# Optimization experiments

Measured on AMD Instinct MI355X. Metric: run time of the kernel, lower is better.

## Reference

```python
import jax, jax.numpy as jnp
import numpy as np

HEADS, MAX_SEQ, N_STATE = 8, 2048, 512
DEPTH = N_STATE // HEADS
B, S = 2, 2048
EPS = 1e-5


def setup_inputs() -> dict:
    key = jax.random.key(0)
    ks = jax.random.split(key, 8)
    sd = lambda f: 1.0 / np.sqrt(f)
    causal = jnp.tril(jnp.ones((S, S), dtype=bool))
    mask = jnp.where(causal, 0.0, -1e9).astype(jnp.float32)[None, None]
    return {
        "x": jax.random.normal(ks[0], (B, S, N_STATE), jnp.float32),
        "mask": mask,
        "W_qkv": jax.random.normal(ks[1], (N_STATE, 3 * N_STATE), jnp.float32) * sd(N_STATE),
        "b_qkv": jnp.zeros((3 * N_STATE,), jnp.float32),
        "W_proj": jax.random.normal(ks[2], (N_STATE, N_STATE), jnp.float32) * sd(N_STATE),
        "b_proj": jnp.zeros((N_STATE,), jnp.float32),
        "E": jax.random.normal(ks[3], (HEADS, MAX_SEQ, DEPTH), jnp.float32) * sd(DEPTH),
        "g1": jnp.ones((N_STATE,), jnp.float32),
        "be1": jnp.zeros((N_STATE,), jnp.float32),
        "g2": jnp.ones((N_STATE,), jnp.float32),
        "be2": jnp.zeros((N_STATE,), jnp.float32),
        "W_fc1": jax.random.normal(ks[4], (N_STATE, 4 * N_STATE), jnp.float32) * sd(N_STATE),
        "b_fc1": jnp.zeros((4 * N_STATE,), jnp.float32),
        "W_fc2": jax.random.normal(ks[5], (4 * N_STATE, N_STATE), jnp.float32) * sd(4 * N_STATE),
        "b_fc2": jnp.zeros((N_STATE,), jnp.float32),
    }


def _layernorm(x, g, b):
    mu = jnp.mean(x, axis=-1, keepdims=True)
    var = jnp.mean(jnp.square(x - mu), axis=-1, keepdims=True)
    return (x - mu) * jax.lax.rsqrt(var + EPS) * g + b


def _relative_skew(rel):
    # rel: [B, H, S, S] = q @ E_slice^T ; skew trick -> relative positions
    b, h, s, _ = rel.shape
    rel = jnp.pad(rel, ((0, 0), (0, 0), (0, 0), (1, 0)))  # [B,H,S,S+1]
    rel = rel.reshape(b, h, s + 1, s)
    return rel[:, :, 1:, :]  # [B,H,S,S]


def reference(x, mask, W_qkv, b_qkv, W_proj, b_proj, E, g1, be1, g2, be2,
              W_fc1, b_fc1, W_fc2, b_fc2):
    b, s, _ = x.shape
    a = _layernorm(x, g1, be1)
    qkv = a @ W_qkv + b_qkv  # [B,S,3N]
    q, k, v = jnp.split(qkv, 3, axis=-1)
    split = lambda t: t.reshape(b, s, HEADS, DEPTH).transpose(0, 2, 1, 3)  # [B,H,S,D]
    q, k, v = split(q), split(k), split(v)
    present = jnp.stack([k, v], axis=1)  # [B,2,H,S,D]

    w = jnp.einsum("bhqd,bhkd->bhqk", q, k)
    E_s = E[:, MAX_SEq if False else MAX_SEQ - s:, :]  # [H,S,D]
    rel = jnp.einsum("bhqd,hld->bhql", q, E_s)
    w = (w + _relative_skew(rel)) * (1.0 / np.sqrt(DEPTH))
    w = w + mask
    w = jax.nn.softmax(w, axis=-1)
    att = jnp.einsum("bhqk,bhkd->bhqd", w, v)
    att = att.transpose(0, 2, 1, 3).reshape(b, s, N_STATE)
    att = att @ W_proj + b_proj

    x = x + att
    m = _layernorm(x, g2, be2)
    m = jax.nn.gelu(m @ W_fc1 + b_fc1) @ W_fc2 + b_fc2
    x = x + m
    return (x, present)
```

## Files before the change

### kernel.cpp

```cpp
#include <hip/hip_runtime.h>
#include <stdint.h>

#define DEV __device__ __forceinline__
#define SCHEDB __builtin_amdgcn_sched_barrier(0)
#define WAITVM(n) asm volatile("s_waitcnt vmcnt(" #n ")" ::: "memory")
#define WAITLG asm volatile("s_waitcnt lgkmcnt(0)" ::: "memory")

typedef __attribute__((ext_vector_type(8))) short bf16x8;
typedef __attribute__((ext_vector_type(4))) float f32x4;

DEV ushort f2bf(float f) {
  union { float f; uint32_t u; } c; c.f = f;
  return (ushort)((c.u + 0x7FFFu + ((c.u >> 16) & 1)) >> 16);
}
DEV bf16x8 ld8(const ushort* p) { return *reinterpret_cast<const bf16x8*>(p); }

DEV void gload16(const void* g, void* l) {
  __builtin_amdgcn_global_load_lds(
      (const __attribute__((address_space(1))) uint32_t*)g,
      (__attribute__((address_space(3))) uint32_t*)l, 16, 0, 0);
}

__global__ __launch_bounds__(256) void k_transpose_bf(const float* __restrict__ in,
                                                      ushort* __restrict__ out,
                                                      int R, int C) {
  __shared__ float t[32][33];
  int tx = threadIdx.x & 31, ty = threadIdx.x >> 5;
  int c0 = blockIdx.x * 32, r0 = blockIdx.y * 32;
#pragma unroll
  for (int k = 0; k < 4; ++k)
    t[ty + 8 * k][tx] = in[(size_t)(r0 + ty + 8 * k) * C + c0 + tx];
  __syncthreads();
#pragma unroll
  for (int k = 0; k < 4; ++k)
    out[(size_t)(c0 + ty + 8 * k) * R + r0 + tx] = f2bf(t[tx][ty + 8 * k]);
}

__global__ __launch_bounds__(256) void k_cvt_bf(const float* __restrict__ in,
                                                ushort* __restrict__ out, int n4) {
  int i = blockIdx.x * 256 + threadIdx.x;
  if (i >= n4) return;
  float4 v = reinterpret_cast<const float4*>(in)[i];
  ushort4 o; o.x = f2bf(v.x); o.y = f2bf(v.y); o.z = f2bf(v.z); o.w = f2bf(v.w);
  reinterpret_cast<ushort4*>(out)[i] = o;
}

__global__ __launch_bounds__(256) void k_ln(const float* __restrict__ x,
                                            const float* __restrict__ g,
                                            const float* __restrict__ be,
                                            ushort* __restrict__ out) {
  int w = threadIdx.x >> 6, lane = threadIdx.x & 63;
  int row = blockIdx.x * 4 + w;
  const float* xr = x + (size_t)row * 512 + lane * 8;
  float4 a = *reinterpret_cast<const float4*>(xr);
  float4 b = *reinterpret_cast<const float4*>(xr + 4);
  float xs[8] = {a.x, a.y, a.z, a.w, b.x, b.y, b.z, b.w};
  float s = 0.f, q = 0.f;
#pragma unroll
  for (int i = 0; i < 8; ++i) { s += xs[i]; q += xs[i] * xs[i]; }
#pragma unroll
  for (int off = 32; off; off >>= 1) { s += __shfl_xor(s, off); q += __shfl_xor(q, off); }
  float mu = s * (1.f / 512.f);
  float var = q * (1.f / 512.f) - mu * mu;
  float inv = rsqrtf(var + 1e-5f);
  const float* gp = g + lane * 8;
  const float* bp = be + lane * 8;
  ushort o[8];
#pragma unroll
  for (int i = 0; i < 8; ++i) o[i] = f2bf((xs[i] - mu) * inv * gp[i] + bp[i]);
  *reinterpret_cast<uint4*>(out + (size_t)row * 512 + lane * 8) = *reinterpret_cast<uint4*>(o);
}

template <int EPI, int BN>
__global__ __launch_bounds__(256) void k_gemm(
    const ushort* __restrict__ A, const ushort* __restrict__ Bt,
    int M, int N, int K,
    const float* __restrict__ bias, const float* __restrict__ res,
    float* __restrict__ outf, ushort* __restrict__ outb,
    float* __restrict__ present, ushort* __restrict__ qbf,
    ushort* __restrict__ kbf, ushort* __restrict__ vtbf) {
  constexpr int NF = BN / 32;
  constexpr int LOADS = 4 + BN / 32;
  __shared__ ushort As[2][128][64];
  __shared__ ushort Bs[2][BN][64];
  const int tid = threadIdx.x, lane = tid & 63, w = tid >> 6;
  const int g = lane >> 4, l16 = lane & 15;
  const int m0 = blockIdx.y * 128, n0 = blockIdx.x * BN;
  const int wm = (w >> 1) * 64, wn = (w & 1) * (BN / 2);
  f32x4 acc[4][NF];
#pragma unroll
  for (int i = 0; i < 4; ++i)
#pragma unroll
    for (int j = 0; j < NF; ++j) acc[i][j] = (f32x4){0.f, 0.f, 0.f, 0.f};

  const int lrow_off = (lane << 4);
  auto stage = [&](int buf, int k0) {
#pragma unroll
    for (int sw = 0; sw < 4; ++sw) {
      int offb = sw * 4096 + w * 1024;
      int loff = offb + lrow_off;
      int row = loff >> 7, colb = loff & 127;
      gload16((const char*)A + (((size_t)(m0 + row) * K + k0) << 1) + colb,
              (char*)(&As[buf][0][0]) + offb);
    }
#pragma unroll
    for (int sw = 0; sw < BN / 32; ++sw) {
      int offb = sw * 4096 + w * 1024;
      int loff = offb + lrow_off;
      int row = loff >> 7, colb = loff & 127;
      gload16((const char*)Bt + (((size_t)(n0 + row) * K + k0) << 1) + colb,
              (char*)(&Bs[buf][0][0]) + offb);
    }
  };

  const int nt = K >> 6;
  stage(0, 0);
  stage(1, 64);
  if constexpr (LOADS == 8) WAITVM(8); else WAITVM(6);
  SCHEDB;
  __builtin_amdgcn_s_barrier();
  SCHEDB;

  for (int t = 0; t < nt; ++t) {
    const int cur = t & 1;
    bf16x8 af[2][4], bfr[2][NF];
#pragma unroll
    for (int kk = 0; kk < 2; ++kk) {
#pragma unroll
      for (int f = 0; f < 4; ++f)
        af[kk][f] = *reinterpret_cast<const bf16x8*>(
            &As[cur][wm + f * 16 + l16][kk * 32 + g * 8]);
#pragma unroll
      for (int f = 0; f < NF; ++f)
        bfr[kk][f] = *reinterpret_cast<const bf16x8*>(
            &Bs[cur][wn + f * 16 + l16][kk * 32 + g * 8]);
    }
    WAITLG;
    SCHEDB;
    __builtin_amdgcn_s_barrier();
    SCHEDB;
    if (t + 2 < nt) stage(cur, (t + 2) << 6);
    SCHEDB;
#pragma unroll
    for (int kk = 0; kk < 2; ++kk)
#pragma unroll
      for (int i = 0; i < 4; ++i)
#pragma unroll
        for (int j = 0; j < NF; ++j)
          acc[i][j] = __builtin_amdgcn_mfma_f32_16x16x32_bf16(
              af[kk][i], bfr[kk][j], acc[i][j], 0, 0, 0);
    SCHEDB;
    if (t + 1 < nt) {
      if (t + 2 < nt) {
        if constexpr (LOADS == 8) WAITVM(8); else WAITVM(6);
      } else {
        WAITVM(0);
      }
      SCHEDB;
      __builtin_amdgcn_s_barrier();
      SCHEDB;
    }
  }

#pragma unroll
  for (int i = 0; i < 4; ++i)
#pragma unroll
    for (int j = 0; j < NF; ++j)
#pragma unroll
      for (int r = 0; r < 4; ++r) {
        int row = m0 + wm + i * 16 + g * 4 + r;
        int col = n0 + wn + j * 16 + l16;
        float v = acc[i][j][r] + bias[col];
        if constexpr (EPI == 0) {
          int third = col >> 9, hh = (col >> 6) & 7, d = col & 63;
          int bb = row >> 11, sq = row & 2047;
          if (third == 0) {
            qbf[((((size_t)bb * 8 + hh) * 2048) + sq) * 64 + d] = f2bf(v);
          } else {
            present[((((size_t)bb * 2 + (third - 1)) * 8 + hh) * 2048 + sq) * 64 + d] = v;
            if (third == 1)
              kbf[((((size_t)bb * 8 + hh) * 2048) + sq) * 64 + d] = f2bf(v);
            else
              vtbf[(((size_t)bb * 8 + hh) * 64 + d) * 2048 + sq] = f2bf(v);
          }
        } else if constexpr (EPI == 1) {
          size_t idx = (size_t)row * N + col;
          outf[idx] = v + res[idx];
        } else {
          float u = 0.7978845608f * (v + 0.044715f * v * v * v);
          float e = __expf(2.f * u);
          float th = 1.f - 2.f / (e + 1.f);
          outb[(size_t)row * N + col] = f2bf(0.5f * v * (1.f + th));
        }
      }
}

__global__ __launch_bounds__(128, 2) void k_attn(
    const ushort* __restrict__ qbf, const ushort* __restrict__ kbf,
    const ushort* __restrict__ vtbf, const ushort* __restrict__ Ebf,
    ushort* __restrict__ attb) {
  constexpr int S = 2048;
  __shared__ ushort Ps[2][16][76];
  __shared__ float Mrg[64][24];
  const int tid = threadIdx.x, lane = tid & 63, ks = tid >> 6;
  const int g = lane >> 4, l16 = lane & 15;
  const int bid = blockIdx.x;
  const int h = bid & 7, rest = bid >> 3;
  const int b = rest & 1, t = 127 - (rest >> 1);
  const int bh = b * 8 + h;

  const ushort* qp = qbf + (size_t)bh * S * 64;
  const ushort* kp = kbf + (size_t)bh * S * 64;
  const ushort* vp = vtbf + (size_t)bh * 64 * S;
  const ushort* ep = Ebf + (size_t)h * S * 64;

  const int i0 = t * 16;
  bf16x8 qf[2];
  qf[0] = ld8(qp + (size_t)(i0 + l16) * 64 + g * 8);
  qf[1] = ld8(qp + (size_t)(i0 + l16) * 64 + 32 + g * 8);
  f32x4 o[4];
#pragma unroll
  for (int fv = 0; fv < 4; ++fv) o[fv] = (f32x4){0.f, 0.f, 0.f, 0.f};
  float mrun[4], lrun[4];
#pragma unroll
  for (int r = 0; r < 4; ++r) { mrun[r] = -1e30f; lrun[r] = 0.f; }
  const int nkt = (t + 4) >> 2;

  for (int kt = ks; kt < nkt; kt += 2) {
    const int j0 = kt * 64;
    const int tb = S - 16 - i0 + j0;
    bf16x8 kf[8], ef[10], vf[8];
#pragma unroll
    for (int fn = 0; fn < 4; ++fn) {
      const ushort* kr = kp + (size_t)(j0 + fn * 16 + l16) * 64 + g * 8;
      kf[fn] = ld8(kr);
      kf[4 + fn] = ld8(kr + 32);
    }
#pragma unroll
    for (int fc = 0; fc < 5; ++fc) {
      int l = tb + fc * 16 + l16; if (l > S - 1) l = S - 1;
      const ushort* er = ep + (size_t)l * 64 + g * 8;
      ef[fc] = ld8(er);
      ef[5 + fc] = ld8(er + 32);
    }
#pragma unroll
    for (int fv = 0; fv < 4; ++fv) {
      const ushort* vr = vp + (size_t)(fv * 16 + l16) * S + j0 + g * 8;
      vf[fv] = ld8(vr);
      vf[4 + fv] = ld8(vr + 32);
    }
    SCHEDB;

    f32x4 sacc[4];
#pragma unroll
    for (int fn = 0; fn < 4; ++fn) sacc[fn] = (f32x4){0.f, 0.f, 0.f, 0.f};
#pragma unroll
    for (int kk = 0; kk < 2; ++kk)
#pragma unroll
      for (int fn = 0; fn < 4; ++fn)
        sacc[fn] = __builtin_amdgcn_mfma_f32_16x16x32_bf16(qf[kk], kf[kk * 4 + fn], sacc[fn], 0, 0, 0);

    f32x4 racc[5];
#pragma unroll
    for (int fc = 0; fc < 5; ++fc) racc[fc] = (f32x4){0.f, 0.f, 0.f, 0.f};
#pragma unroll
    for (int kk = 0; kk < 2; ++kk)
#pragma unroll
      for (int fc = 0; fc < 5; ++fc)
        racc[fc] = __builtin_amdgcn_mfma_f32_16x16x32_bf16(qf[kk], ef[kk * 5 + fc], racc[fc], 0, 0, 0);

    float Sv[4][4], mtile[4];
#pragma unroll
    for (int r = 0; r < 4; ++r) mtile[r] = -1e30f;
#pragma unroll
    for (int r = 0; r < 4; ++r) {
      const int dr = g * 4 + r;
      const int src = (lane & 48) | ((l16 + 15 - dr) & 15);
      const bool hi = (l16 > dr);
#pragma unroll
      for (int fn = 0; fn < 4; ++fn) {
        float lo_v = __shfl(racc[fn][r], src);
        float hi_v = __shfl(racc[fn + 1][r], src);
        float rel = hi ? hi_v : lo_v;
        float sv = (sacc[fn][r] + rel) * 0.125f;
        int dj = fn * 16 + l16;
        if (j0 + dj > i0 + dr) sv = -1e30f;
        Sv[fn][r] = sv;
        mtile[r] = fmaxf(mtile[r], sv);
      }
    }
#pragma unroll
    for (int off = 1; off < 16; off <<= 1)
#pragma unroll
      for (int r = 0; r < 4; ++r) mtile[r] = fmaxf(mtile[r], __shfl_xor(mtile[r], off));
    float corr[4], psum[4];
#pragma unroll
    for (int r = 0; r < 4; ++r) {
      float mn = fmaxf(mrun[r], mtile[r]);
      corr[r] = __expf(mrun[r] - mn);
      mrun[r] = mn;
      psum[r] = 0.f;
    }
#pragma unroll
    for (int fn = 0; fn < 4; ++fn)
#pragma unroll
      for (int r = 0; r < 4; ++r) {
        float pv = __expf(Sv[fn][r] - mrun[r]);
        psum[r] += pv;
        Ps[ks][g * 4 + r][fn * 16 + l16] = f2bf(pv);
      }
#pragma unroll
    for (int off = 1; off < 16; off <<= 1)
#pragma unroll
      for (int r = 0; r < 4; ++r) psum[r] += __shfl_xor(psum[r], off);
#pragma unroll
    for (int r = 0; r < 4; ++r) lrun[r] = lrun[r] * corr[r] + psum[r];
#pragma unroll
    for (int fv = 0; fv < 4; ++fv)
#pragma unroll
      for (int r = 0; r < 4; ++r) o[fv][r] *= corr[r];

#pragma unroll
    for (int kk = 0; kk < 2; ++kk) {
      bf16x8 pf = ld8(&Ps[ks][l16][kk * 32 + g * 8]);
#pragma unroll
      for (int fv = 0; fv < 4; ++fv)
        o[fv] = __builtin_amdgcn_mfma_f32_16x16x32_bf16(pf, vf[kk * 4 + fv], o[fv], 0, 0, 0);
    }
  }

  if (ks == 1) {
    float* mb = &Mrg[lane][0];
#pragma unroll
    for (int fv = 0; fv < 4; ++fv)
#pragma unroll
      for (int r = 0; r < 4; ++r) mb[fv * 4 + r] = o[fv][r];
#pragma unroll
    for (int r = 0; r < 4; ++r) { mb[16 + r] = mrun[r]; mb[20 + r] = lrun[r]; }
  }
  __syncthreads();
  if (ks == 0) {
    const float* mb = &Mrg[lane][0];
#pragma unroll
    for (int r = 0; r < 4; ++r) {
      float m1 = mb[16 + r];
      float mm = fmaxf(mrun[r], m1);
      float e0 = __expf(mrun[r] - mm), e1 = __expf(m1 - mm);
      float lc = lrun[r] * e0 + mb[20 + r] * e1;
      float inv = 1.f / lc;
#pragma unroll
      for (int fv = 0; fv < 4; ++fv) {
        float oc = o[fv][r] * e0 + mb[fv * 4 + r] * e1;
        attb[(size_t)(b * S + i0 + g * 4 + r) * 512 + h * 64 + fv * 16 + l16] =
            f2bf(oc * inv);
      }
    }
  }
}

extern "C" void kernel_launch(void* const* d_in, const int* in_sizes, int n_in,
                              void* d_out, int out_size, void* d_ws, size_t ws_size,
                              hipStream_t stream) {
  const float* x = (const float*)d_in[0];
  const float* W_qkv = (const float*)d_in[2];
  const float* b_qkv = (const float*)d_in[3];
  const float* W_proj = (const float*)d_in[4];
  const float* b_proj = (const float*)d_in[5];
  const float* E = (const float*)d_in[6];
  const float* g1 = (const float*)d_in[7];
  const float* be1 = (const float*)d_in[8];
  const float* g2 = (const float*)d_in[9];
  const float* be2 = (const float*)d_in[10];
  const float* W_fc1 = (const float*)d_in[11];
  const float* b_fc1 = (const float*)d_in[12];
  const float* W_fc2 = (const float*)d_in[13];
  const float* b_fc2 = (const float*)d_in[14];

  float* x_out = (float*)d_out;
  float* present = x_out + 2097152;

  char* ws = (char*)d_ws;
  ushort* a_bf   = (ushort*)(ws + 0);
  ushort* m_bf   = (ushort*)(ws + 4194304);
  ushort* q_bf   = (ushort*)(ws + 8388608);
  ushort* att_bf = (ushort*)(ws + 12582912);
  ushort* h_bf   = (ushort*)(ws + 16777216);
  ushort* k_bf   = (ushort*)(ws + 16777216);
  ushort* vt_bf  = (ushort*)(ws + 20971520);
  float*  x2     = (float*)(ws + 33554432);
  ushort* Wqkv_t = (ushort*)(ws + 41943040);
  ushort* Wproj_t= (ushort*)(ws + 43515904);
  ushort* Wfc1_t = (ushort*)(ws + 44040192);
  ushort* Wfc2_t = (ushort*)(ws + 46137344);
  ushort* E_bf   = (ushort*)(ws + 48234496);

  k_transpose_bf<<<dim3(48, 16), 256, 0, stream>>>(W_qkv, Wqkv_t, 512, 1536);
  k_transpose_bf<<<dim3(16, 16), 256, 0, stream>>>(W_proj, Wproj_t, 512, 512);
  k_transpose_bf<<<dim3(64, 16), 256, 0, stream>>>(W_fc1, Wfc1_t, 512, 2048);
  k_transpose_bf<<<dim3(16, 64), 256, 0, stream>>>(W_fc2, Wfc2_t, 2048, 512);
  k_cvt_bf<<<1024, 256, 0, stream>>>(E, E_bf, 262144);
  k_ln<<<1024, 256, 0, stream>>>(x, g1, be1, a_bf);
  k_gemm<0, 128><<<dim3(12, 32), 256, 0, stream>>>(a_bf, Wqkv_t, 4096, 1536, 512,
                                                   b_qkv, nullptr, nullptr, nullptr,
                                                   present, q_bf, k_bf, vt_bf);
  k_attn<<<2048, 128, 0, stream>>>(q_bf, k_bf, vt_bf, E_bf, att_bf);
  k_gemm<1, 64><<<dim3(8, 32), 256, 0, stream>>>(att_bf, Wproj_t, 4096, 512, 512,
                                                 b_proj, x, x2, nullptr, nullptr, nullptr,
                                                 nullptr, nullptr);
  k_ln<<<1024, 256, 0, stream>>>(x2, g2, be2, m_bf);
  k_gemm<2, 128><<<dim3(16, 32), 256, 0, stream>>>(m_bf, Wfc1_t, 4096, 2048, 512,
                                                   b_fc1, nullptr, nullptr, h_bf, nullptr,
                                                   nullptr, nullptr, nullptr);
  k_gemm<1, 64><<<dim3(8, 32), 256, 0, stream>>>(h_bf, Wfc2_t, 4096, 512, 2048,
                                                 b_fc2, x2, x_out, nullptr, nullptr, nullptr,
                                                 nullptr, nullptr);
}
```

Measured before the change: 312.1 us.

## Share K/V/E tiles in LDS across four query-row waves in attention

The attention kernel now processes 64 query rows per 256-thread block, with each wave owning 16 rows. K, V and relative-embedding tiles are staged once into swizzled, double-buffered LDS with async global-to-LDS loads and shared by all four waves, where before each wave loaded them from global memory on its own. The old split of keys across two waves and the LDS merge of partial softmax states is removed, so each wave walks the full key range by itself. This cuts redundant global traffic but adds per-tile barriers, uses more LDS, and shortens the grid, with coarser causal load balancing.

```diff
diff --git a/kernel.cpp b/kernel.cpp
--- a/kernel.cpp
+++ b/kernel.cpp
@@ -80,7 +80,6 @@
     float* __restrict__ present, ushort* __restrict__ qbf,
     ushort* __restrict__ kbf, ushort* __restrict__ vtbf) {
   constexpr int NF = BN / 32;
-  constexpr int LOADS = 4 + BN / 32;
   __shared__ ushort As[2][128][64];
   __shared__ ushort Bs[2][BN][64];
   const int tid = threadIdx.x, lane = tid & 63, w = tid >> 6;
@@ -116,7 +115,7 @@
   const int nt = K >> 6;
   stage(0, 0);
   stage(1, 64);
-  if constexpr (LOADS == 8) WAITVM(8); else WAITVM(6);
+  if constexpr (BN == 128) WAITVM(8); else WAITVM(6);
   SCHEDB;
   __builtin_amdgcn_s_barrier();
   SCHEDB;
@@ -152,7 +151,7 @@
     SCHEDB;
     if (t + 1 < nt) {
       if (t + 2 < nt) {
-        if constexpr (LOADS == 8) WAITVM(8); else WAITVM(6);
+        if constexpr (BN == 128) WAITVM(8); else WAITVM(6);
       } else {
         WAITVM(0);
       }
@@ -195,18 +194,20 @@
       }
 }
 
-__global__ __launch_bounds__(128, 2) void k_attn(
+__global__ __launch_bounds__(256, 2) void k_attn(
     const ushort* __restrict__ qbf, const ushort* __restrict__ kbf,
     const ushort* __restrict__ vtbf, const ushort* __restrict__ Ebf,
     ushort* __restrict__ attb) {
   constexpr int S = 2048;
-  __shared__ ushort Ps[2][16][76];
-  __shared__ float Mrg[64][24];
-  const int tid = threadIdx.x, lane = tid & 63, ks = tid >> 6;
+  __shared__ ushort Ks[2][64][64];
+  __shared__ ushort Vs[2][64][64];
+  __shared__ ushort Es[2][128][64];
+  __shared__ ushort Ps[4][16][76];
+  const int tid = threadIdx.x, lane = tid & 63, w = tid >> 6;
   const int g = lane >> 4, l16 = lane & 15;
   const int bid = blockIdx.x;
   const int h = bid & 7, rest = bid >> 3;
-  const int b = rest & 1, t = 127 - (rest >> 1);
+  const int b = rest & 1, tq = 31 - (rest >> 1);
   const int bh = b * 8 + h;
 
   const ushort* qp = qbf + (size_t)bh * S * 64;
@@ -214,42 +215,60 @@
   const ushort* vp = vtbf + (size_t)bh * 64 * S;
   const ushort* ep = Ebf + (size_t)h * S * 64;
 
-  const int i0 = t * 16;
+  const int i0 = tq * 64;
+  const int iw = i0 + w * 16;
+  const int rbase = 48 - w * 16;
+
   bf16x8 qf[2];
-  qf[0] = ld8(qp + (size_t)(i0 + l16) * 64 + g * 8);
-  qf[1] = ld8(qp + (size_t)(i0 + l16) * 64 + 32 + g * 8);
+  qf[0] = ld8(qp + (size_t)(iw + l16) * 64 + g * 8);
+  qf[1] = ld8(qp + (size_t)(iw + l16) * 64 + 32 + g * 8);
   f32x4 o[4];
 #pragma unroll
   for (int fv = 0; fv < 4; ++fv) o[fv] = (f32x4){0.f, 0.f, 0.f, 0.f};
   float mrun[4], lrun[4];
 #pragma unroll
   for (int r = 0; r < 4; ++r) { mrun[r] = -1e30f; lrun[r] = 0.f; }
-  const int nkt = (t + 4) >> 2;
-
-  for (int kt = ks; kt < nkt; kt += 2) {
+  const int nkt = tq + 1;
+
+  auto stage = [&](int buf, int kt) {
     const int j0 = kt * 64;
-    const int tb = S - 16 - i0 + j0;
-    bf16x8 kf[8], ef[10], vf[8];
-#pragma unroll
-    for (int fn = 0; fn < 4; ++fn) {
-      const ushort* kr = kp + (size_t)(j0 + fn * 16 + l16) * 64 + g * 8;
-      kf[fn] = ld8(kr);
-      kf[4 + fn] = ld8(kr + 32);
-    }
-#pragma unroll
-    for (int fc = 0; fc < 5; ++fc) {
-      int l = tb + fc * 16 + l16; if (l > S - 1) l = S - 1;
-      const ushort* er = ep + (size_t)l * 64 + g * 8;
-      ef[fc] = ld8(er);
-      ef[5 + fc] = ld8(er + 32);
-    }
-#pragma unroll
-    for (int fv = 0; fv < 4; ++fv) {
-      const ushort* vr = vp + (size_t)(fv * 16 + l16) * S + j0 + g * 8;
-      vf[fv] = ld8(vr);
-      vf[4 + fv] = ld8(vr + 32);
-    }
-    SCHEDB;
+    const int ebase = S - 64 - i0 + j0;
+#pragma unroll
+    for (int c = 0; c < 2; ++c) {
+      int chunk = w * 2 + c;
+      int row = chunk * 8 + (lane >> 3);
+      int ccp = (lane & 7) ^ (row & 7);
+      gload16(kp + (size_t)(j0 + row) * 64 + ccp * 8,
+              (char*)(&Ks[buf][0][0]) + chunk * 1024);
+      gload16(vp + (size_t)row * S + j0 + ccp * 8,
+              (char*)(&Vs[buf][0][0]) + chunk * 1024);
+    }
+#pragma unroll
+    for (int c = 0; c < 4; ++c) {
+      int chunk = w * 4 + c;
+      int row = chunk * 8 + (lane >> 3);
+      int l = ebase + row;
+      l = l < 0 ? 0 : (l > S - 1 ? S - 1 : l);
+      int ccp = (lane & 7) ^ (row & 7);
+      gload16(ep + (size_t)l * 64 + ccp * 8,
+              (char*)(&Es[buf][0][0]) + chunk * 1024);
+    }
+  };
+
+  stage(0, 0);
+  WAITVM(0);
+  SCHEDB;
+  __builtin_amdgcn_s_barrier();
+  SCHEDB;
+
+  for (int kt = 0; kt < nkt; ++kt) {
+    const int cur = kt & 1;
+    const int j0 = kt * 64;
+    if (kt + 1 < nkt) stage(cur ^ 1, kt + 1);
+    SCHEDB;
+    const char* KsB = (const char*)&Ks[cur][0][0];
+    const char* VsB = (const char*)&Vs[cur][0][0];
+    const char* EsB = (const char*)&Es[cur][0][0];
 
     f32x4 sacc[4];
 #pragma unroll
@@ -257,17 +276,22 @@
 #pragma unroll
     for (int kk = 0; kk < 2; ++kk)
 #pragma unroll
-      for (int fn = 0; fn < 4; ++fn)
-        sacc[fn] = __builtin_amdgcn_mfma_f32_16x16x32_bf16(qf[kk], kf[kk * 4 + fn], sacc[fn], 0, 0, 0);
-
+      for (int fn = 0; fn < 4; ++fn) {
+        int row = fn * 16 + l16, chunk = kk * 4 + g;
+        bf16x8 kfr = ld8((const ushort*)(KsB + row * 128 + (((chunk ^ (row & 7))) << 4)));
+        sacc[fn] = __builtin_amdgcn_mfma_f32_16x16x32_bf16(qf[kk], kfr, sacc[fn], 0, 0, 0);
+      }
     f32x4 racc[5];
 #pragma unroll
     for (int fc = 0; fc < 5; ++fc) racc[fc] = (f32x4){0.f, 0.f, 0.f, 0.f};
 #pragma unroll
     for (int kk = 0; kk < 2; ++kk)
 #pragma unroll
-      for (int fc = 0; fc < 5; ++fc)
-        racc[fc] = __builtin_amdgcn_mfma_f32_16x16x32_bf16(qf[kk], ef[kk * 5 + fc], racc[fc], 0, 0, 0);
+      for (int fc = 0; fc < 5; ++fc) {
+        int row = rbase + fc * 16 + l16, chunk = kk * 4 + g;
+        bf16x8 efr = ld8((const ushort*)(EsB + row * 128 + (((chunk ^ (row & 7))) << 4)));
+        racc[fc] = __builtin_amdgcn_mfma_f32_16x16x32_bf16(qf[kk], efr, racc[fc], 0, 0, 0);
+      }
 
     float Sv[4][4], mtile[4];
 #pragma unroll
@@ -284,7 +308,7 @@
         float rel = hi ? hi_v : lo_v;
         float sv = (sacc[fn][r] + rel) * 0.125f;
         int dj = fn * 16 + l16;
-        if (j0 + dj > i0 + dr) sv = -1e30f;
+        if (j0 + dj > iw + dr) sv = -1e30f;
         Sv[fn][r] = sv;
         mtile[r] = fmaxf(mtile[r], sv);
       }
@@ -307,7 +331,7 @@
       for (int r = 0; r < 4; ++r) {
         float pv = __expf(Sv[fn][r] - mrun[r]);
         psum[r] += pv;
-        Ps[ks][g * 4 + r][fn * 16 + l16] = f2bf(pv);
+        Ps[w][g * 4 + r][fn * 16 + l16] = f2bf(pv);
       }
 #pragma unroll
     for (int off = 1; off < 16; off <<= 1)
@@ -322,40 +346,31 @@
 
 #pragma unroll
     for (int kk = 0; kk < 2; ++kk) {
-      bf16x8 pf = ld8(&Ps[ks][l16][kk * 32 + g * 8]);
-#pragma unroll
-      for (int fv = 0; fv < 4; ++fv)
-        o[fv] = __builtin_amdgcn_mfma_f32_16x16x32_bf16(pf, vf[kk * 4 + fv], o[fv], 0, 0, 0);
+      bf16x8 pf = ld8(&Ps[w][l16][kk * 32 + g * 8]);
+#pragma unroll
+      for (int fv = 0; fv < 4; ++fv) {
+        int row = fv * 16 + l16, chunk = kk * 4 + g;
+        bf16x8 vfr = ld8((const ushort*)(VsB + row * 128 + (((chunk ^ (row & 7))) << 4)));
+        o[fv] = __builtin_amdgcn_mfma_f32_16x16x32_bf16(pf, vfr, o[fv], 0, 0, 0);
+      }
+    }
+    SCHEDB;
+    if (kt + 1 < nkt) {
+      WAITVM(0);
+      SCHEDB;
+      __builtin_amdgcn_s_barrier();
+      SCHEDB;
     }
   }
 
-  if (ks == 1) {
-    float* mb = &Mrg[lane][0];
-#pragma unroll
-    for (int fv = 0; fv < 4; ++fv)
-#pragma unroll
-      for (int r = 0; r < 4; ++r) mb[fv * 4 + r] = o[fv][r];
-#pragma unroll
-    for (int r = 0; r < 4; ++r) { mb[16 + r] = mrun[r]; mb[20 + r] = lrun[r]; }
-  }
-  __syncthreads();
-  if (ks == 0) {
-    const float* mb = &Mrg[lane][0];
+#pragma unroll
+  for (int fv = 0; fv < 4; ++fv)
 #pragma unroll
     for (int r = 0; r < 4; ++r) {
-      float m1 = mb[16 + r];
-      float mm = fmaxf(mrun[r], m1);
-      float e0 = __expf(mrun[r] - mm), e1 = __expf(m1 - mm);
-      float lc = lrun[r] * e0 + mb[20 + r] * e1;
-      float inv = 1.f / lc;
-#pragma unroll
-      for (int fv = 0; fv < 4; ++fv) {
-        float oc = o[fv][r] * e0 + mb[fv * 4 + r] * e1;
-        attb[(size_t)(b * S + i0 + g * 4 + r) * 512 + h * 64 + fv * 16 + l16] =
-            f2bf(oc * inv);
-      }
-    }
-  }
+      int dr = g * 4 + r;
+      float v = o[fv][r] / lrun[r];
+      attb[(size_t)(b * S + iw + dr) * 512 + h * 64 + fv * 16 + l16] = f2bf(v);
+    }
 }
 
 extern "C" void kernel_launch(void* const* d_in, const int* in_sizes, int n_in,
@@ -403,7 +418,7 @@
   k_gemm<0, 128><<<dim3(12, 32), 256, 0, stream>>>(a_bf, Wqkv_t, 4096, 1536, 512,
                                                    b_qkv, nullptr, nullptr, nullptr,
                                                    present, q_bf, k_bf, vt_bf);
-  k_attn<<<2048, 128, 0, stream>>>(q_bf, k_bf, vt_bf, E_bf, att_bf);
+  k_attn<<<512, 256, 0, stream>>>(q_bf, k_bf, vt_bf, E_bf, att_bf);
   k_gemm<1, 64><<<dim3(8, 32), 256, 0, stream>>>(att_bf, Wproj_t, 4096, 512, 512,
                                                  b_proj, x, x2, nullptr, nullptr, nullptr,
                                                  nullptr, nullptr);
```

Result: faster. 290.1 us (-7.0%).
